# Kernel tuning notes

Measured on AMD Instinct MI355X. Metric: run time of the kernel, lower is better.

Reference implementation:

```python
import jax, jax.numpy as jnp
import numpy as np

N = 50000      # nodes
E = 800000     # edges
G = 64         # graphs in batch
IN_F, H1, C1, C2, OUT_F = 128, 4, 32, 64, 16
D1 = H1 * C1   # 128, concat output of gat1
EPS = 1e-5
NEG_SLOPE = 0.2


def setup_inputs() -> dict:
    key = jax.random.key(0)
    ks = jax.random.split(key, 16)
    rn = lambda k, shape, s=0.1: jax.random.normal(k, shape, jnp.float32) * s
    inp = {
        'x': jax.random.normal(ks[0], (N, IN_F), jnp.float32),
        'edge_index': jax.random.randint(ks[1], (2, E), 0, N),
        'edge_attr': jax.random.uniform(ks[2], (E, 1), jnp.float32),
        'batch': jnp.sort(jax.random.randint(ks[3], (N,), 0, G)),
        # GATv2 layer 1 (heads=4, concat)
        'Wl1': rn(ks[4], (IN_F, D1)), 'bl1': jnp.zeros((D1,), jnp.float32),
        'Wr1': rn(ks[5], (IN_F, D1)), 'br1': jnp.zeros((D1,), jnp.float32),
        'We1': rn(ks[6], (1, D1)), 'att1': rn(ks[7], (H1, C1)),
        'bias1': jnp.zeros((D1,), jnp.float32),
        # GATv2 layer 2 (heads=1, concat=False)
        'Wl2': rn(ks[8], (D1, C2)), 'bl2': jnp.zeros((C2,), jnp.float32),
        'Wr2': rn(ks[9], (D1, C2)), 'br2': jnp.zeros((C2,), jnp.float32),
        'We2': rn(ks[10], (1, C2)), 'att2': rn(ks[11], (1, C2)),
        'bias2': jnp.zeros((C2,), jnp.float32),
        # batchnorms
        'bn1_gamma': jnp.ones((D1,), jnp.float32), 'bn1_beta': jnp.zeros((D1,), jnp.float32),
        'bn2_gamma': jnp.ones((C2,), jnp.float32), 'bn2_beta': jnp.zeros((C2,), jnp.float32),
        # final linear over [sum|mean|max] pooled features
        'Wlin': rn(ks[12], (3 * C2, OUT_F)), 'blin': jnp.zeros((OUT_F,), jnp.float32),
    }
    return inp


def gatv2(x, src, dst, edge_attr, Wl, bl, Wr, br, We, att, bias, H, C, concat):
    n = x.shape[0]
    xl = (x @ Wl + bl).reshape(n, H, C)          # source transform (lin_l)
    xr = (x @ Wr + br).reshape(n, H, C)          # target transform (lin_r)
    e = (edge_attr @ We).reshape(-1, H, C)       # edge transform (lin_edge)
    m = jax.nn.leaky_relu(xl[src] + xr[dst] + e, NEG_SLOPE)  # [E,H,C]
    alpha = jnp.einsum('ehc,hc->eh', m, att)     # attention logits [E,H]
    amax = jax.ops.segment_max(alpha, dst, num_segments=n)
    amax = jnp.where(jnp.isfinite(amax), amax, 0.0)
    p = jnp.exp(alpha - amax[dst])
    denom = jax.ops.segment_sum(p, dst, num_segments=n)
    a = p / (denom[dst] + 1e-16)                 # per-destination softmax
    out = jax.ops.segment_sum(xl[src] * a[:, :, None], dst, num_segments=n)
    out = out.reshape(n, H * C) if concat else out.mean(axis=1)
    return out + bias


def batchnorm(x, gamma, beta):
    mu = x.mean(axis=0)
    var = x.var(axis=0)  # biased var, as torch BN uses for normalization
    return (x - mu) * jax.lax.rsqrt(var + EPS) * gamma + beta


def reference(x, edge_index, edge_attr, batch,
              Wl1, bl1, Wr1, br1, We1, att1, bias1,
              Wl2, bl2, Wr2, br2, We2, att2, bias2,
              bn1_gamma, bn1_beta, bn2_gamma, bn2_beta,
              Wlin, blin):
    src, dst = edge_index[0], edge_index[1]
    h = jax.nn.relu(gatv2(x, src, dst, edge_attr, Wl1, bl1, Wr1, br1, We1, att1, bias1, H1, C1, True))
    h = batchnorm(h, bn1_gamma, bn1_beta)
    # dropout omitted (eval-mode reference)
    h = jax.nn.relu(gatv2(h, src, dst, edge_attr, Wl2, bl2, Wr2, br2, We2, att2, bias2, 1, C2, False))
    h = batchnorm(h, bn2_gamma, bn2_beta)
    # multi-pool over graphs
    s = jax.ops.segment_sum(h, batch, num_segments=G)
    cnt = jax.ops.segment_sum(jnp.ones((h.shape[0], 1), h.dtype), batch, num_segments=G)
    mean = s / jnp.maximum(cnt, 1.0)
    mx = jax.ops.segment_max(h, batch, num_segments=G)
    feat = jnp.concatenate([s, mean, mx], axis=-1)   # [G, 3*C2]
    return feat @ Wlin + blin
```

## Files before the change

kernel.cpp:

```cpp
#include <hip/hip_runtime.h>
#include <math.h>


typedef __attribute__((ext_vector_type(8))) short short8v;
typedef __attribute__((ext_vector_type(8))) unsigned short ushort8v;
typedef __attribute__((ext_vector_type(4))) unsigned short ushort4v;
typedef __attribute__((ext_vector_type(4))) float f32x4v;

#define BUCKCAP 8192

__device__ __forceinline__ void atomicMaxFloat(float* addr, float val) {
    if (val >= 0.f) atomicMax((int*)addr, __float_as_int(val));
    else            atomicMin((unsigned int*)addr, __float_as_uint(val));
}
__device__ __forceinline__ void atomicMinFloat(float* addr, float val) {
    if (val >= 0.f) atomicMin((int*)addr, __float_as_int(val));
    else            atomicMax((unsigned int*)addr, __float_as_uint(val));
}

__device__ __forceinline__ unsigned short f2bf(float f) {
    unsigned u = __float_as_uint(f);
    unsigned r = u + 0x7FFFu + ((u >> 16) & 1u);
    return (unsigned short)(r >> 16);
}
__device__ __forceinline__ float bf2f(unsigned short h) {
    return __uint_as_float((unsigned)h << 16);
}

__global__ void setup_kernel(const float* __restrict__ x,
                             const float* __restrict__ Wl1, const float* __restrict__ Wr1,
                             unsigned short* __restrict__ xbf, unsigned short* __restrict__ w1t,
                             int* __restrict__ bcur, float* __restrict__ bn1stats,
                             float* __restrict__ bn2stats, float* __restrict__ gsum,
                             float* __restrict__ gmax, float* __restrict__ gmin,
                             float* __restrict__ gcnt, int nquads) {
    int i = blockIdx.x * blockDim.x + threadIdx.x;
    int stride = gridDim.x * blockDim.x;
    for (int j = i; j < nquads; j += stride) {
        float4 v = ((const float4*)x)[j];
        ushort4 o = { f2bf(v.x), f2bf(v.y), f2bf(v.z), f2bf(v.w) };
        ((ushort4*)xbf)[j] = o;
    }
    for (int j = i; j < 256 * 128; j += stride) {
        int col = j >> 7, k = j & 127;
        float w = (col < 128) ? Wl1[k * 128 + col] : Wr1[k * 128 + (col - 128)];
        w1t[j] = f2bf(w);
    }
    for (int j = i; j < 64 * 64; j += stride) { gsum[j] = 0.f; gmax[j] = -INFINITY; gmin[j] = INFINITY; }
    if (i < 256) { bcur[i] = 0; bn1stats[i] = 0.f; }
    if (i < 128) bn2stats[i] = 0.f;
    if (i < 64)  gcnt[i] = 0.f;
}

__global__ __launch_bounds__(256)
void passA_kernel(const int* __restrict__ esrc_in, const int* __restrict__ edst_in,
                  const float* __restrict__ eattr, uint2* __restrict__ brec,
                  int* __restrict__ bcur, int nE) {
    __shared__ unsigned scnt[256];
    __shared__ unsigned sbase[256];
    const int t = threadIdx.x;
    const int e0 = blockIdx.x * 4096;
    scnt[t] = 0;
    __syncthreads();
    unsigned rx[16], ry[16]; unsigned short rk[16];
#pragma unroll
    for (int j = 0; j < 16; ++j) {
        int e = e0 + j * 256 + t;
        if (e < nE) {
            unsigned d = (unsigned)edst_in[e];
            rx[j] = (d << 16) | (unsigned)esrc_in[e];
            ry[j] = __float_as_uint(eattr[e]);
            rk[j] = (unsigned short)atomicAdd(&scnt[d >> 8], 1u);
        }
    }
    __syncthreads();
    sbase[t] = (scnt[t] > 0) ? (unsigned)atomicAdd(&bcur[t], (int)scnt[t]) : 0u;
    __syncthreads();
#pragma unroll
    for (int j = 0; j < 16; ++j) {
        int e = e0 + j * 256 + t;
        if (e < nE) {
            unsigned b = rx[j] >> 24;
            unsigned pos = sbase[b] + rk[j];
            if (pos < BUCKCAP) brec[(size_t)b * BUCKCAP + pos] = make_uint2(rx[j], ry[j]);
        }
    }
}

__global__ __launch_bounds__(256)
void passB1_kernel(const uint2* __restrict__ brec, const int* __restrict__ bcur,
                   int* __restrict__ deg, int nN) {
    __shared__ unsigned cnt[256];
    const int b = blockIdx.x, t = threadIdx.x;
    cnt[t] = 0;
    __syncthreads();
    const int n = bcur[b];
    const uint2* r = brec + (size_t)b * BUCKCAP;
    for (int i = t; i < n; i += 256) atomicAdd(&cnt[(r[i].x >> 16) & 255u], 1u);
    __syncthreads();
    const int d0 = b << 8;
    if (d0 + t < nN) deg[d0 + t] = (int)cnt[t];
}

__global__ void scan1_kernel(const int* __restrict__ deg, int* __restrict__ rowptr,
                             int* __restrict__ bsum, int n) {
    __shared__ int buf[1024];
    int t = threadIdx.x;
    int i = blockIdx.x * 1024 + t;
    int v = (i < n) ? deg[i] : 0;
    buf[t] = v;
    __syncthreads();
    for (int off = 1; off < 1024; off <<= 1) {
        int xv = (t >= off) ? buf[t - off] : 0;
        __syncthreads();
        buf[t] += xv;
        __syncthreads();
    }
    if (i < n) rowptr[i] = buf[t] - v;
    if (t == 1023) bsum[blockIdx.x] = buf[1023];
}

__global__ void scan3_kernel(int* __restrict__ rowptr, const int* __restrict__ bsum,
                             int n, int nE) {
    __shared__ int spref;
    int t = threadIdx.x;
    if (t < 64) {
        int acc = 0;
        for (int i = t; i < blockIdx.x; i += 64) acc += bsum[i];
#pragma unroll
        for (int off = 32; off; off >>= 1) acc += __shfl_xor(acc, off);
        if (t == 0) spref = acc;
    }
    __syncthreads();
    int i = blockIdx.x * 1024 + t;
    if (i < n) rowptr[i] += spref;
    if (i == 0) rowptr[n] = nE;
}

__global__ __launch_bounds__(256)
void passB2_kernel(const uint2* __restrict__ brec, const int* __restrict__ bcur,
                   const int* __restrict__ rowptr, unsigned* __restrict__ edges, int nN) {
    __shared__ unsigned cur[256];
    __shared__ int rp[256];
    const int b = blockIdx.x, t = threadIdx.x;
    const int d0 = b << 8;
    cur[t] = 0;
    if (d0 + t < nN) rp[t] = rowptr[d0 + t];
    __syncthreads();
    const int n = bcur[b];
    const uint2* r = brec + (size_t)b * BUCKCAP;
    for (int i = t; i < n; i += 256) {
        uint2 rec = r[i];
        unsigned dlo = (rec.x >> 16) & 255u;
        unsigned rank = atomicAdd(&cur[dlo], 1u);
        int pos = rp[dlo] + (int)rank;
        edges[pos] = (rec.x & 0xFFFFu) | ((unsigned)f2bf(__uint_as_float(rec.y)) << 16);
    }
}

template <int NO>
__global__ __launch_bounds__(256)
void mfma_transform_kernel(const unsigned short* __restrict__ A,
                           const unsigned short* __restrict__ Wt,
                           const float* __restrict__ bL, const float* __restrict__ bR,
                           unsigned short* __restrict__ outL, unsigned short* __restrict__ outR,
                           int M) {
    constexpr int NCG = NO / 64;
    const int wid  = (blockIdx.x * blockDim.x + threadIdx.x) >> 6;
    const int lane = threadIdx.x & 63;
    const int rowblk = wid / NCG;
    const int cg     = wid % NCG;
    if (rowblk * 16 >= M) return;
    int r = rowblk * 16 + (lane & 15);
    if (r >= M) r = M - 1;
    const int ko = (lane >> 4) * 8;
    const int cbase = cg * 64;

    f32x4v acc0 = {0.f,0.f,0.f,0.f}, acc1 = acc0, acc2 = acc0, acc3 = acc0;
#pragma unroll
    for (int k0 = 0; k0 < 128; k0 += 32) {
        short8v a = *(const short8v*)(A + (size_t)r * 128 + k0 + ko);
        const unsigned short* wp = Wt + (size_t)(cbase + (lane & 15)) * 128 + k0 + ko;
        short8v b0 = *(const short8v*)(wp);
        short8v b1 = *(const short8v*)(wp + 16 * 128);
        short8v b2 = *(const short8v*)(wp + 32 * 128);
        short8v b3 = *(const short8v*)(wp + 48 * 128);
        acc0 = __builtin_amdgcn_mfma_f32_16x16x32_bf16(a, b0, acc0, 0, 0, 0);
        acc1 = __builtin_amdgcn_mfma_f32_16x16x32_bf16(a, b1, acc1, 0, 0, 0);
        acc2 = __builtin_amdgcn_mfma_f32_16x16x32_bf16(a, b2, acc2, 0, 0, 0);
        acc3 = __builtin_amdgcn_mfma_f32_16x16x32_bf16(a, b3, acc3, 0, 0, 0);
    }

    const int colL  = lane & 15;
    const int rquad = (lane >> 4) * 4;
    f32x4v accs[4] = { acc0, acc1, acc2, acc3 };
#pragma unroll
    for (int c = 0; c < 4; ++c) {
        const int gcol = cbase + c * 16 + colL;
        float bias; unsigned short* outp; int oc;
        if (gcol < NO / 2) { bias = bL[gcol]; outp = outL; oc = gcol; }
        else               { bias = bR[gcol - NO / 2]; outp = outR; oc = gcol - NO / 2; }
#pragma unroll
        for (int j = 0; j < 4; ++j) {
            const int row = rowblk * 16 + rquad + j;
            if (row < M) outp[(size_t)row * (NO / 2) + oc] = f2bf(accs[c][j] + bias);
        }
    }
}

__global__ __launch_bounds__(256)
void gather1_kernel(const unsigned short* __restrict__ xl, const unsigned short* __restrict__ xr,
                    const int* __restrict__ rowptr, const unsigned* __restrict__ edges,
                    const float* __restrict__ We, const float* __restrict__ att,
                    const float* __restrict__ bias, unsigned short* __restrict__ y, int nN) {
    const int lane = threadIdx.x & 63;
    const int sub  = lane >> 4;
    const int sl   = lane & 15;
    const int c0   = sl * 8;
    const int waveg = (blockIdx.x * blockDim.x + threadIdx.x) >> 6;
    const int n = waveg * 4 + sub;
    const bool valid = (n < nN);

    float xrv[8];
    int ks = 0, ke = 0;
    if (valid) {
        ushort8v xu = *(const ushort8v*)(xr + (size_t)n * 128 + c0);
#pragma unroll
        for (int j = 0; j < 8; ++j) xrv[j] = bf2f(xu[j]);
        ks = rowptr[n]; ke = rowptr[n + 1];
    } else {
#pragma unroll
        for (int j = 0; j < 8; ++j) xrv[j] = 0.f;
    }
    const float4 we0 = *(const float4*)(We + c0);
    const float4 we1 = *(const float4*)(We + c0 + 4);
    const float4 at0 = *(const float4*)(att + c0);
    const float4 at1 = *(const float4*)(att + c0 + 4);
    const float wev[8] = { we0.x, we0.y, we0.z, we0.w, we1.x, we1.y, we1.z, we1.w };
    const float atv[8] = { at0.x, at0.y, at0.z, at0.w, at1.x, at1.y, at1.z, at1.w };

    float d = 0.f, a[8];
#pragma unroll
    for (int j = 0; j < 8; ++j) a[j] = 0.f;

    for (int kb = ks; __any(kb < ke); kb += 16) {
        unsigned ew = 0;
        if (kb + sl < ke) ew = edges[kb + sl];
        const int cnt = ke - kb;
        for (int j = 0; j < 16; j += 2) {
            const bool a0 = j < cnt, a1 = (j + 1) < cnt;
            if (!__any(a0)) break;
            const unsigned w0 = __shfl(ew, sub * 16 + j);
            const unsigned w1 = __shfl(ew, sub * 16 + j + 1);
            const int s0 = w0 & 0xFFFFu, s1 = w1 & 0xFFFFu;
            const ushort8v xu0 = *(const ushort8v*)(xl + (size_t)s0 * 128 + c0);
            const ushort8v xu1 = *(const ushort8v*)(xl + (size_t)s1 * 128 + c0);
            const float ea0 = bf2f((unsigned short)(w0 >> 16));
            const float ea1 = bf2f((unsigned short)(w1 >> 16));
            float xv0[8], xv1[8], p0 = 0.f, p1 = 0.f;
#pragma unroll
            for (int q = 0; q < 8; ++q) {
                xv0[q] = bf2f(xu0[q]);
                float tq = xv0[q] + xrv[q] + ea0 * wev[q];
                tq = fmaxf(tq, 0.2f * tq);
                p0 += tq * atv[q];
                xv1[q] = bf2f(xu1[q]);
                float uq = xv1[q] + xrv[q] + ea1 * wev[q];
                uq = fmaxf(uq, 0.2f * uq);
                p1 += uq * atv[q];
            }
            p0 += __shfl_xor(p0, 1); p0 += __shfl_xor(p0, 2);
            p1 += __shfl_xor(p1, 1); p1 += __shfl_xor(p1, 2);
            const float e0v = a0 ? __expf(p0) : 0.f;
            const float e1v = a1 ? __expf(p1) : 0.f;
            d += e0v + e1v;
#pragma unroll
            for (int q = 0; q < 8; ++q) a[q] += e0v * xv0[q] + e1v * xv1[q];
        }
    }
    if (valid) {
        const float inv = 1.f / (d + 1e-16f);
        ushort8v o;
#pragma unroll
        for (int j = 0; j < 8; ++j) o[j] = f2bf(fmaxf(a[j] * inv + bias[c0 + j], 0.f));
        *(ushort8v*)(y + (size_t)n * 128 + c0) = o;
    }
}

__global__ __launch_bounds__(256)
void gather2_kernel(const unsigned short* __restrict__ xl, const unsigned short* __restrict__ xr,
                    const int* __restrict__ rowptr, const unsigned* __restrict__ edges,
                    const float* __restrict__ We, const float* __restrict__ att,
                    const float* __restrict__ bias, float* __restrict__ y, int nN) {
    const int lane = threadIdx.x & 63;
    const int sub  = lane >> 4;
    const int sl   = lane & 15;
    const int c0   = sl * 4;
    const int waveg = (blockIdx.x * blockDim.x + threadIdx.x) >> 6;
    const int n = waveg * 4 + sub;
    const bool valid = (n < nN);

    float xrv[4];
    int ks = 0, ke = 0;
    if (valid) {
        ushort4v xu = *(const ushort4v*)(xr + (size_t)n * 64 + c0);
#pragma unroll
        for (int j = 0; j < 4; ++j) xrv[j] = bf2f(xu[j]);
        ks = rowptr[n]; ke = rowptr[n + 1];
    } else {
#pragma unroll
        for (int j = 0; j < 4; ++j) xrv[j] = 0.f;
    }
    const float4 wev4 = *(const float4*)(We + c0);
    const float4 atv4 = *(const float4*)(att + c0);
    const float wev[4] = { wev4.x, wev4.y, wev4.z, wev4.w };
    const float atv[4] = { atv4.x, atv4.y, atv4.z, atv4.w };

    float d = 0.f, a[4] = {0.f, 0.f, 0.f, 0.f};
    for (int kb = ks; __any(kb < ke); kb += 16) {
        unsigned ew = 0;
        if (kb + sl < ke) ew = edges[kb + sl];
        const int cnt = ke - kb;
        for (int j = 0; j < 16; j += 2) {
            const bool a0 = j < cnt, a1 = (j + 1) < cnt;
            if (!__any(a0)) break;
            const unsigned w0 = __shfl(ew, sub * 16 + j);
            const unsigned w1 = __shfl(ew, sub * 16 + j + 1);
            const int s0 = w0 & 0xFFFFu, s1 = w1 & 0xFFFFu;
            const ushort4v xu0 = *(const ushort4v*)(xl + (size_t)s0 * 64 + c0);
            const ushort4v xu1 = *(const ushort4v*)(xl + (size_t)s1 * 64 + c0);
            const float ea0 = bf2f((unsigned short)(w0 >> 16));
            const float ea1 = bf2f((unsigned short)(w1 >> 16));
            float xv0[4], xv1[4], p0 = 0.f, p1 = 0.f;
#pragma unroll
            for (int q = 0; q < 4; ++q) {
                xv0[q] = bf2f(xu0[q]);
                float tq = xv0[q] + xrv[q] + ea0 * wev[q];
                tq = fmaxf(tq, 0.2f * tq);
                p0 += tq * atv[q];
                xv1[q] = bf2f(xu1[q]);
                float uq = xv1[q] + xrv[q] + ea1 * wev[q];
                uq = fmaxf(uq, 0.2f * uq);
                p1 += uq * atv[q];
            }
            p0 += __shfl_xor(p0, 1); p0 += __shfl_xor(p0, 2);
            p0 += __shfl_xor(p0, 4); p0 += __shfl_xor(p0, 8);
            p1 += __shfl_xor(p1, 1); p1 += __shfl_xor(p1, 2);
            p1 += __shfl_xor(p1, 4); p1 += __shfl_xor(p1, 8);
            const float e0v = a0 ? __expf(p0) : 0.f;
            const float e1v = a1 ? __expf(p1) : 0.f;
            d += e0v + e1v;
#pragma unroll
            for (int q = 0; q < 4; ++q) a[q] += e0v * xv0[q] + e1v * xv1[q];
        }
    }
    if (valid) {
        const float inv = 1.f / (d + 1e-16f);
        float4 o;
        o.x = fmaxf(a[0] * inv + bias[c0],     0.f);
        o.y = fmaxf(a[1] * inv + bias[c0 + 1], 0.f);
        o.z = fmaxf(a[2] * inv + bias[c0 + 2], 0.f);
        o.w = fmaxf(a[3] * inv + bias[c0 + 3], 0.f);
        *(float4*)(y + (size_t)n * 64 + c0) = o;
    }
}

__global__ void bn_stats_bf128_kernel(const unsigned short* __restrict__ y,
                                      float* __restrict__ stats, int rows) {
    const int t = threadIdx.x;
    const int col = t & 127;
    const int rsub = t >> 7;
    float s = 0.f, q = 0.f;
    for (int r = blockIdx.x * 2 + rsub; r < rows; r += gridDim.x * 2) {
        float v = bf2f(y[(size_t)r * 128 + col]);
        s += v; q += v * v;
    }
    atomicAdd(&stats[col], s);
    atomicAdd(&stats[128 + col], q);
}

__global__ void wfold2_kernel(const float* __restrict__ Wl2, const float* __restrict__ bl2,
                              const float* __restrict__ Wr2, const float* __restrict__ br2,
                              const float* __restrict__ stats, const float* __restrict__ gamma,
                              const float* __restrict__ beta,
                              unsigned short* __restrict__ w2t, float* __restrict__ b2f, int nN) {
    __shared__ float sc[128], sh[128];
    const int t = threadIdx.x;
    if (t < 128) {
        float invN = 1.f / nN;
        float mu = stats[t] * invN;
        float var = stats[128 + t] * invN - mu * mu;
        float k = gamma[t] * rsqrtf(var + 1e-5f);
        sc[t] = k; sh[t] = beta[t] - mu * k;
    }
    __syncthreads();
    if (t < 128) {
        const int oc = (t < 64) ? t : t - 64;
        const float* W = (t < 64) ? Wl2 : Wr2;
        float acc = (t < 64) ? bl2[oc] : br2[oc];
        for (int k = 0; k < 128; ++k) acc += sh[k] * W[k * 64 + oc];
        b2f[t] = acc;
    }
    for (int i = t; i < 128 * 128; i += 256) {
        int col = i >> 7, k = i & 127;
        const int oc = (col < 64) ? col : col - 64;
        const float* W = (col < 64) ? Wl2 : Wr2;
        w2t[i] = f2bf(sc[k] * W[k * 64 + oc]);
    }
}

__global__ void pool_kernel(const float* __restrict__ y2, const int* __restrict__ batch,
                            float* __restrict__ gsum, float* __restrict__ gmax,
                            float* __restrict__ gmin, float* __restrict__ gcnt,
                            float* __restrict__ bn2stats, int rows) {
    const int t = threadIdx.x;
    const int col = t & 63;
    const int rsub = t >> 6;
    const int base = blockIdx.x * 256;
    int curg = -1; float s = 0.f, mx = 0.f, mn = 0.f, cnt = 0.f;
    float bs = 0.f, bq = 0.f;
    int rend = rows < base + 256 ? rows : base + 256;
    for (int r = base + rsub; r < rend; r += 4) {
        int g = batch[r];
        float v = y2[(size_t)r * 64 + col];
        bs += v; bq += v * v;
        if (g != curg) {
            if (curg >= 0) {
                atomicAdd(&gsum[curg * 64 + col], s);
                atomicMaxFloat(&gmax[curg * 64 + col], mx);
                atomicMinFloat(&gmin[curg * 64 + col], mn);
                if (col == 0) atomicAdd(&gcnt[curg], cnt);
            }
            curg = g; s = v; mx = v; mn = v; cnt = 1.f;
        } else {
            s += v; mx = fmaxf(mx, v); mn = fminf(mn, v); cnt += 1.f;
        }
    }
    if (curg >= 0) {
        atomicAdd(&gsum[curg * 64 + col], s);
        atomicMaxFloat(&gmax[curg * 64 + col], mx);
        atomicMinFloat(&gmin[curg * 64 + col], mn);
        if (col == 0) atomicAdd(&gcnt[curg], cnt);
    }
    __shared__ float red[2][4][64];
    red[0][rsub][col] = bs; red[1][rsub][col] = bq;
    __syncthreads();
    if (rsub == 0) {
        float ts = red[0][0][col] + red[0][1][col] + red[0][2][col] + red[0][3][col];
        float tq = red[1][0][col] + red[1][1][col] + red[1][2][col] + red[1][3][col];
        atomicAdd(&bn2stats[col], ts);
        atomicAdd(&bn2stats[64 + col], tq);
    }
}

__global__ void final_kernel(const float* __restrict__ gsum, const float* __restrict__ gmax,
                             const float* __restrict__ gmin, const float* __restrict__ gcnt,
                             const float* __restrict__ bn2stats, const float* __restrict__ gamma,
                             const float* __restrict__ beta, const float* __restrict__ Wlin,
                             const float* __restrict__ blin, float* __restrict__ out, int nN) {
    __shared__ float feat[64][192];
    __shared__ float sc[64], sh[64];
    int t = threadIdx.x;
    if (t < 64) {
        float invN = 1.f / nN;
        float mu = bn2stats[t] * invN;
        float var = bn2stats[64 + t] * invN - mu * mu;
        float k = gamma[t] * rsqrtf(var + 1e-5f);
        sc[t] = k; sh[t] = beta[t] - mu * k;
    }
    __syncthreads();
    for (int i = t; i < 64 * 64; i += 256) {
        int g = i >> 6, c = i & 63;
        float cntg = gcnt[g];
        float s_bn = sc[c] * gsum[i] + sh[c] * cntg;
        feat[g][c]       = s_bn;
        feat[g][64 + c]  = s_bn / fmaxf(cntg, 1.f);
        feat[g][128 + c] = (sc[c] >= 0.f) ? sc[c] * gmax[i] + sh[c]
                                          : sc[c] * gmin[i] + sh[c];
    }
    __syncthreads();
    for (int i = t; i < 64 * 16; i += 256) {
        int g = i >> 4, j = i & 15;
        float acc = blin[j];
        for (int k = 0; k < 192; ++k) acc += feat[g][k] * Wlin[k * 16 + j];
        out[g * 16 + j] = acc;
    }
}

extern "C" void kernel_launch(void* const* d_in, const int* in_sizes, int n_in,
                              void* d_out, int out_size, void* d_ws, size_t ws_size,
                              hipStream_t stream) {
    const float* x     = (const float*)d_in[0];
    const int*   eidx  = (const int*)d_in[1];
    const float* eattr = (const float*)d_in[2];
    const int*   batch = (const int*)d_in[3];
    const float* Wl1 = (const float*)d_in[4];  const float* bl1 = (const float*)d_in[5];
    const float* Wr1 = (const float*)d_in[6];  const float* br1 = (const float*)d_in[7];
    const float* We1 = (const float*)d_in[8];  const float* att1 = (const float*)d_in[9];
    const float* bias1 = (const float*)d_in[10];
    const float* Wl2 = (const float*)d_in[11]; const float* bl2 = (const float*)d_in[12];
    const float* Wr2 = (const float*)d_in[13]; const float* br2 = (const float*)d_in[14];
    const float* We2 = (const float*)d_in[15]; const float* att2 = (const float*)d_in[16];
    const float* bias2 = (const float*)d_in[17];
    const float* g1 = (const float*)d_in[18];  const float* b1 = (const float*)d_in[19];
    const float* g2 = (const float*)d_in[20];  const float* b2 = (const float*)d_in[21];
    const float* Wlin = (const float*)d_in[22]; const float* blin = (const float*)d_in[23];
    float* out = (float*)d_out;

    const int nN = in_sizes[0] / 128;
    const int nE = in_sizes[1] / 2;
    const int* esrc_in = eidx;
    const int* edst_in = eidx + nE;
    const int nbuck = (nN + 255) >> 8;

    char* ws = (char*)d_ws;
    size_t o = 0;
    auto alloc = [&](size_t bytes) { size_t r = o; o += (bytes + 255) & ~(size_t)255; return r; };
    unsigned short* B0 = (unsigned short*)(ws + alloc((size_t)nN * 128 * 2));
    unsigned short* B1 = (unsigned short*)(ws + alloc((size_t)nN * 128 * 2));
    char*           B2 = (char*)(ws + alloc((size_t)nN * 128 * 2));
    unsigned short* w1t = (unsigned short*)(ws + alloc(256 * 128 * 2));
    unsigned short* w2t = (unsigned short*)(ws + alloc(128 * 128 * 2));
    float* b2f    = (float*)(ws + alloc(128 * 4));
    uint2* brec   = (uint2*)(ws + alloc((size_t)nbuck * BUCKCAP * 8));
    unsigned* edges = (unsigned*)(ws + alloc((size_t)nE * 4));
    int*   bcur   = (int*)(ws + alloc(256 * 4));
    int*   rowptr = (int*)(ws + alloc((size_t)(nN + 1) * 4));
    int*   deg    = (int*)(ws + alloc((size_t)nN * 4));
    int*   bsum   = (int*)(ws + alloc(256 * 4));
    float* bn1stats = (float*)(ws + alloc(256 * 4));
    float* bn2stats = (float*)(ws + alloc(128 * 4));
    float* gsum = (float*)(ws + alloc(64 * 64 * 4));
    float* gmax = (float*)(ws + alloc(64 * 64 * 4));
    float* gmin = (float*)(ws + alloc(64 * 64 * 4));
    float* gcnt = (float*)(ws + alloc(64 * 4));

    unsigned short* xbf  = B0;
    unsigned short* y1bf = B0;
    unsigned short* xl1b = B1;
    unsigned short* xr1b = (unsigned short*)B2;
    unsigned short* xl2b = B1;
    unsigned short* xr2b = B1 + (size_t)nN * 64;
    float*          y2   = (float*)B2;

    const int nScanBlocks = (nN + 1023) / 1024;
    const int mBlk = (nN + 15) / 16;
    const int t1Blocks = mBlk;
    const int t2Blocks = (mBlk * 2 + 3) / 4;

    setup_kernel<<<2048, 256, 0, stream>>>(x, Wl1, Wr1, xbf, w1t, bcur,
                                           bn1stats, bn2stats, gsum, gmax, gmin, gcnt, nN * 32);
    passA_kernel<<<(nE + 4095) / 4096, 256, 0, stream>>>(esrc_in, edst_in, eattr, brec, bcur, nE);
    passB1_kernel<<<nbuck, 256, 0, stream>>>(brec, bcur, deg, nN);
    scan1_kernel<<<nScanBlocks, 1024, 0, stream>>>(deg, rowptr, bsum, nN);
    scan3_kernel<<<nScanBlocks, 1024, 0, stream>>>(rowptr, bsum, nN, nE);
    passB2_kernel<<<nbuck, 256, 0, stream>>>(brec, bcur, rowptr, edges, nN);

    mfma_transform_kernel<256><<<t1Blocks, 256, 0, stream>>>(
        xbf, w1t, bl1, br1, xl1b, xr1b, nN);
    gather1_kernel<<<(nN + 15) / 16, 256, 0, stream>>>(
        xl1b, xr1b, rowptr, edges, We1, att1, bias1, y1bf, nN);
    bn_stats_bf128_kernel<<<256, 256, 0, stream>>>(y1bf, bn1stats, nN);
    wfold2_kernel<<<1, 256, 0, stream>>>(Wl2, bl2, Wr2, br2, bn1stats, g1, b1, w2t, b2f, nN);

    mfma_transform_kernel<128><<<t2Blocks, 256, 0, stream>>>(
        y1bf, w2t, b2f, b2f + 64, xl2b, xr2b, nN);
    gather2_kernel<<<(nN + 15) / 16, 256, 0, stream>>>(
        xl2b, xr2b, rowptr, edges, We2, att2, bias2, y2, nN);

    pool_kernel<<<(nN + 255) / 256, 256, 0, stream>>>(y2, batch, gsum, gmax, gmin, gcnt, bn2stats, nN);
    final_kernel<<<1, 256, 0, stream>>>(gsum, gmax, gmin, gcnt, bn2stats, g2, b2, Wlin, blin, out, nN);
}
```

Baseline: 369.0 us.

## Fuse degree count and row-pointer scan into bucket pass; unroll gathers by four

The bucket degree-count kernel now computes each bucket's global offset by reducing the preceding bucket totals, then does a local exclusive scan and writes rowptr directly. This removes two separate scan kernels, their launches and the deg and bsum buffers. Both gather kernels now process four edges per inner step instead of two, issuing four independent row loads before computing, to expose more memory-level parallelism. In exchange, each bucket block redundantly reduces up to 256 counts, and the wider unroll raises register pressure.

```diff
diff --git a/kernel.cpp b/kernel.cpp
--- a/kernel.cpp
+++ b/kernel.cpp
@@ -89,52 +89,35 @@
 
 __global__ __launch_bounds__(256)
 void passB1_kernel(const uint2* __restrict__ brec, const int* __restrict__ bcur,
-                   int* __restrict__ deg, int nN) {
+                   int* __restrict__ rowptr, int nN, int nE) {
     __shared__ unsigned cnt[256];
+    __shared__ int red[256];
     const int b = blockIdx.x, t = threadIdx.x;
     cnt[t] = 0;
-    __syncthreads();
+    red[t] = (t < b) ? bcur[t] : 0;
+    __syncthreads();
+    for (int off = 128; off; off >>= 1) {
+        if (t < off) red[t] += red[t + off];
+        __syncthreads();
+    }
+    const int base = red[0];
     const int n = bcur[b];
     const uint2* r = brec + (size_t)b * BUCKCAP;
     for (int i = t; i < n; i += 256) atomicAdd(&cnt[(r[i].x >> 16) & 255u], 1u);
     __syncthreads();
-    const int d0 = b << 8;
-    if (d0 + t < nN) deg[d0 + t] = (int)cnt[t];
-}
-
-__global__ void scan1_kernel(const int* __restrict__ deg, int* __restrict__ rowptr,
-                             int* __restrict__ bsum, int n) {
-    __shared__ int buf[1024];
-    int t = threadIdx.x;
-    int i = blockIdx.x * 1024 + t;
-    int v = (i < n) ? deg[i] : 0;
-    buf[t] = v;
-    __syncthreads();
-    for (int off = 1; off < 1024; off <<= 1) {
-        int xv = (t >= off) ? buf[t - off] : 0;
+    const unsigned v = cnt[t];
+    red[t] = (int)v;
+    __syncthreads();
+    for (int off = 1; off < 256; off <<= 1) {
+        int xv = (t >= off) ? red[t - off] : 0;
         __syncthreads();
-        buf[t] += xv;
+        red[t] += xv;
         __syncthreads();
     }
-    if (i < n) rowptr[i] = buf[t] - v;
-    if (t == 1023) bsum[blockIdx.x] = buf[1023];
-}
-
-__global__ void scan3_kernel(int* __restrict__ rowptr, const int* __restrict__ bsum,
-                             int n, int nE) {
-    __shared__ int spref;
-    int t = threadIdx.x;
-    if (t < 64) {
-        int acc = 0;
-        for (int i = t; i < blockIdx.x; i += 64) acc += bsum[i];
-#pragma unroll
-        for (int off = 32; off; off >>= 1) acc += __shfl_xor(acc, off);
-        if (t == 0) spref = acc;
-    }
-    __syncthreads();
-    int i = blockIdx.x * 1024 + t;
-    if (i < n) rowptr[i] += spref;
-    if (i == 0) rowptr[n] = nE;
+    const int excl = red[t] - (int)v;
+    const int d = (b << 8) + t;
+    if (d <= nN) rowptr[d] = base + excl;
+    if (b == gridDim.x - 1 && t == 255) rowptr[nN] = nE;
 }
 
 __global__ __launch_bounds__(256)
@@ -208,6 +191,42 @@
     }
 }
 
+__device__ __forceinline__ float edge_c8(unsigned w, bool act, ushort8v xu,
+                                         const float* xrv, const float* wev,
+                                         const float* atv, float* xv) {
+    const float ea = bf2f((unsigned short)(w >> 16));
+    float part = 0.f;
+#pragma unroll
+    for (int q = 0; q < 8; ++q) {
+        xv[q] = bf2f(xu[q]);
+        float t = xv[q] + xrv[q] + ea * wev[q];
+        t = fmaxf(t, 0.2f * t);
+        part += t * atv[q];
+    }
+    part += __shfl_xor(part, 1);
+    part += __shfl_xor(part, 2);
+    return act ? __expf(part) : 0.f;
+}
+
+__device__ __forceinline__ float edge_c4(unsigned w, bool act, ushort4v xu,
+                                         const float* xrv, const float* wev,
+                                         const float* atv, float* xv) {
+    const float ea = bf2f((unsigned short)(w >> 16));
+    float part = 0.f;
+#pragma unroll
+    for (int q = 0; q < 4; ++q) {
+        xv[q] = bf2f(xu[q]);
+        float t = xv[q] + xrv[q] + ea * wev[q];
+        t = fmaxf(t, 0.2f * t);
+        part += t * atv[q];
+    }
+    part += __shfl_xor(part, 1);
+    part += __shfl_xor(part, 2);
+    part += __shfl_xor(part, 4);
+    part += __shfl_xor(part, 8);
+    return act ? __expf(part) : 0.f;
+}
+
 __global__ __launch_bounds__(256)
 void gather1_kernel(const unsigned short* __restrict__ xl, const unsigned short* __restrict__ xr,
                     const int* __restrict__ rowptr, const unsigned* __restrict__ edges,
@@ -244,38 +263,29 @@
     for (int j = 0; j < 8; ++j) a[j] = 0.f;
 
     for (int kb = ks; __any(kb < ke); kb += 16) {
-        unsigned ew = 0;
-        if (kb + sl < ke) ew = edges[kb + sl];
+        const unsigned ew = (kb + sl < ke) ? edges[kb + sl] : 0u;
         const int cnt = ke - kb;
-        for (int j = 0; j < 16; j += 2) {
-            const bool a0 = j < cnt, a1 = (j + 1) < cnt;
-            if (!__any(a0)) break;
-            const unsigned w0 = __shfl(ew, sub * 16 + j);
+        for (int j = 0; j < 16; j += 4) {
+            if (!__any(j < cnt)) break;
+            const unsigned w0 = __shfl(ew, sub * 16 + j + 0);
             const unsigned w1 = __shfl(ew, sub * 16 + j + 1);
-            const int s0 = w0 & 0xFFFFu, s1 = w1 & 0xFFFFu;
-            const ushort8v xu0 = *(const ushort8v*)(xl + (size_t)s0 * 128 + c0);
-            const ushort8v xu1 = *(const ushort8v*)(xl + (size_t)s1 * 128 + c0);
-            const float ea0 = bf2f((unsigned short)(w0 >> 16));
-            const float ea1 = bf2f((unsigned short)(w1 >> 16));
-            float xv0[8], xv1[8], p0 = 0.f, p1 = 0.f;
-#pragma unroll
-            for (int q = 0; q < 8; ++q) {
-                xv0[q] = bf2f(xu0[q]);
-                float tq = xv0[q] + xrv[q] + ea0 * wev[q];
-                tq = fmaxf(tq, 0.2f * tq);
-                p0 += tq * atv[q];
-                xv1[q] = bf2f(xu1[q]);
-                float uq = xv1[q] + xrv[q] + ea1 * wev[q];
-                uq = fmaxf(uq, 0.2f * uq);
-                p1 += uq * atv[q];
-            }
-            p0 += __shfl_xor(p0, 1); p0 += __shfl_xor(p0, 2);
-            p1 += __shfl_xor(p1, 1); p1 += __shfl_xor(p1, 2);
-            const float e0v = a0 ? __expf(p0) : 0.f;
-            const float e1v = a1 ? __expf(p1) : 0.f;
-            d += e0v + e1v;
-#pragma unroll
-            for (int q = 0; q < 8; ++q) a[q] += e0v * xv0[q] + e1v * xv1[q];
+            const unsigned w2 = __shfl(ew, sub * 16 + j + 2);
+            const unsigned w3 = __shfl(ew, sub * 16 + j + 3);
+            const ushort8v xu0 = *(const ushort8v*)(xl + (size_t)(w0 & 0xFFFFu) * 128 + c0);
+            const ushort8v xu1 = *(const ushort8v*)(xl + (size_t)(w1 & 0xFFFFu) * 128 + c0);
+            const ushort8v xu2 = *(const ushort8v*)(xl + (size_t)(w2 & 0xFFFFu) * 128 + c0);
+            const ushort8v xu3 = *(const ushort8v*)(xl + (size_t)(w3 & 0xFFFFu) * 128 + c0);
+            float xva[8], xvb[8];
+            const float e0 = edge_c8(w0, j + 0 < cnt, xu0, xrv, wev, atv, xva);
+            const float e1 = edge_c8(w1, j + 1 < cnt, xu1, xrv, wev, atv, xvb);
+            d += e0 + e1;
+#pragma unroll
+            for (int q = 0; q < 8; ++q) a[q] += e0 * xva[q] + e1 * xvb[q];
+            const float e2 = edge_c8(w2, j + 2 < cnt, xu2, xrv, wev, atv, xva);
+            const float e3 = edge_c8(w3, j + 3 < cnt, xu3, xrv, wev, atv, xvb);
+            d += e2 + e3;
+#pragma unroll
+            for (int q = 0; q < 8; ++q) a[q] += e2 * xva[q] + e3 * xvb[q];
         }
     }
     if (valid) {
@@ -318,40 +328,29 @@
 
     float d = 0.f, a[4] = {0.f, 0.f, 0.f, 0.f};
     for (int kb = ks; __any(kb < ke); kb += 16) {
-        unsigned ew = 0;
-        if (kb + sl < ke) ew = edges[kb + sl];
+        const unsigned ew = (kb + sl < ke) ? edges[kb + sl] : 0u;
         const int cnt = ke - kb;
-        for (int j = 0; j < 16; j += 2) {
-            const bool a0 = j < cnt, a1 = (j + 1) < cnt;
-            if (!__any(a0)) break;
-            const unsigned w0 = __shfl(ew, sub * 16 + j);
+        for (int j = 0; j < 16; j += 4) {
+            if (!__any(j < cnt)) break;
+            const unsigned w0 = __shfl(ew, sub * 16 + j + 0);
             const unsigned w1 = __shfl(ew, sub * 16 + j + 1);
-            const int s0 = w0 & 0xFFFFu, s1 = w1 & 0xFFFFu;
-            const ushort4v xu0 = *(const ushort4v*)(xl + (size_t)s0 * 64 + c0);
-            const ushort4v xu1 = *(const ushort4v*)(xl + (size_t)s1 * 64 + c0);
-            const float ea0 = bf2f((unsigned short)(w0 >> 16));
-            const float ea1 = bf2f((unsigned short)(w1 >> 16));
-            float xv0[4], xv1[4], p0 = 0.f, p1 = 0.f;
-#pragma unroll
-            for (int q = 0; q < 4; ++q) {
-                xv0[q] = bf2f(xu0[q]);
-                float tq = xv0[q] + xrv[q] + ea0 * wev[q];
-                tq = fmaxf(tq, 0.2f * tq);
-                p0 += tq * atv[q];
-                xv1[q] = bf2f(xu1[q]);
-                float uq = xv1[q] + xrv[q] + ea1 * wev[q];
-                uq = fmaxf(uq, 0.2f * uq);
-                p1 += uq * atv[q];
-            }
-            p0 += __shfl_xor(p0, 1); p0 += __shfl_xor(p0, 2);
-            p0 += __shfl_xor(p0, 4); p0 += __shfl_xor(p0, 8);
-            p1 += __shfl_xor(p1, 1); p1 += __shfl_xor(p1, 2);
-            p1 += __shfl_xor(p1, 4); p1 += __shfl_xor(p1, 8);
-            const float e0v = a0 ? __expf(p0) : 0.f;
-            const float e1v = a1 ? __expf(p1) : 0.f;
-            d += e0v + e1v;
-#pragma unroll
-            for (int q = 0; q < 4; ++q) a[q] += e0v * xv0[q] + e1v * xv1[q];
+            const unsigned w2 = __shfl(ew, sub * 16 + j + 2);
+            const unsigned w3 = __shfl(ew, sub * 16 + j + 3);
+            const ushort4v xu0 = *(const ushort4v*)(xl + (size_t)(w0 & 0xFFFFu) * 64 + c0);
+            const ushort4v xu1 = *(const ushort4v*)(xl + (size_t)(w1 & 0xFFFFu) * 64 + c0);
+            const ushort4v xu2 = *(const ushort4v*)(xl + (size_t)(w2 & 0xFFFFu) * 64 + c0);
+            const ushort4v xu3 = *(const ushort4v*)(xl + (size_t)(w3 & 0xFFFFu) * 64 + c0);
+            float xva[4], xvb[4];
+            const float e0 = edge_c4(w0, j + 0 < cnt, xu0, xrv, wev, atv, xva);
+            const float e1 = edge_c4(w1, j + 1 < cnt, xu1, xrv, wev, atv, xvb);
+            d += e0 + e1;
+#pragma unroll
+            for (int q = 0; q < 4; ++q) a[q] += e0 * xva[q] + e1 * xvb[q];
+            const float e2 = edge_c4(w2, j + 2 < cnt, xu2, xrv, wev, atv, xva);
+            const float e3 = edge_c4(w3, j + 3 < cnt, xu3, xrv, wev, atv, xvb);
+            d += e2 + e3;
+#pragma unroll
+            for (int q = 0; q < 4; ++q) a[q] += e2 * xva[q] + e3 * xvb[q];
         }
     }
     if (valid) {
@@ -526,8 +525,6 @@
     unsigned* edges = (unsigned*)(ws + alloc((size_t)nE * 4));
     int*   bcur   = (int*)(ws + alloc(256 * 4));
     int*   rowptr = (int*)(ws + alloc((size_t)(nN + 1) * 4));
-    int*   deg    = (int*)(ws + alloc((size_t)nN * 4));
-    int*   bsum   = (int*)(ws + alloc(256 * 4));
     float* bn1stats = (float*)(ws + alloc(256 * 4));
     float* bn2stats = (float*)(ws + alloc(128 * 4));
     float* gsum = (float*)(ws + alloc(64 * 64 * 4));
@@ -543,7 +540,6 @@
     unsigned short* xr2b = B1 + (size_t)nN * 64;
     float*          y2   = (float*)B2;
 
-    const int nScanBlocks = (nN + 1023) / 1024;
     const int mBlk = (nN + 15) / 16;
     const int t1Blocks = mBlk;
     const int t2Blocks = (mBlk * 2 + 3) / 4;
@@ -551,9 +547,7 @@
     setup_kernel<<<2048, 256, 0, stream>>>(x, Wl1, Wr1, xbf, w1t, bcur,
                                            bn1stats, bn2stats, gsum, gmax, gmin, gcnt, nN * 32);
     passA_kernel<<<(nE + 4095) / 4096, 256, 0, stream>>>(esrc_in, edst_in, eattr, brec, bcur, nE);
-    passB1_kernel<<<nbuck, 256, 0, stream>>>(brec, bcur, deg, nN);
-    scan1_kernel<<<nScanBlocks, 1024, 0, stream>>>(deg, rowptr, bsum, nN);
-    scan3_kernel<<<nScanBlocks, 1024, 0, stream>>>(rowptr, bsum, nN, nE);
+    passB1_kernel<<<nbuck, 256, 0, stream>>>(brec, bcur, rowptr, nN, nE);
     passB2_kernel<<<nbuck, 256, 0, stream>>>(brec, bcur, rowptr, edges, nN);
 
     mfma_transform_kernel<256><<<t1Blocks, 256, 0, stream>>>(
```

Result: no change. 364.1 us (-1.3%).
